# Kernel optimization log

Measured on AMD Instinct MI355X. Metric: run time of the kernel, lower is better.

## Reference

```python
import jax, jax.numpy as jnp
import numpy as np

NEG_INF = -9e15
ALPHA = 0.2  # attention leaky_relu slope


def _gat_layer(h, adj_mask, W, a1, a2):
    # h: [N, Fin], W: [Fin, D], a1/a2: [D]
    Wh = h @ W                                   # [N, D]
    f1 = Wh @ a1                                 # [N]
    f2 = Wh @ a2                                 # [N]
    e = jax.nn.leaky_relu(f1[:, None] + f2[None, :], ALPHA)  # [N, N]
    scores = jnp.where(adj_mask, e, NEG_INF)
    att = jax.nn.softmax(scores, axis=-1)        # row-normalized over neighbors
    return att @ Wh                              # [N, D]


def setup_inputs() -> dict:
    key = jax.random.key(0)
    ks = jax.random.split(key, 12)
    N, Fin, H, D, C = 4096, 512, 8, 64, 64
    s = 0.1
    x = jax.random.normal(ks[0], (N, Fin), jnp.float32)
    adj = jax.random.randint(ks[1], (N, N), 0, 2, jnp.int32)
    W = jax.random.normal(ks[2], (H, Fin, D), jnp.float32) * s
    a1 = jax.random.normal(ks[3], (H, D), jnp.float32) * s
    a2 = jax.random.normal(ks[4], (H, D), jnp.float32) * s
    Wo = jax.random.normal(ks[5], (H * D, C), jnp.float32) * s
    ao1 = jax.random.normal(ks[6], (C,), jnp.float32) * s
    ao2 = jax.random.normal(ks[7], (C,), jnp.float32) * s
    W1 = jax.random.normal(ks[8], (512, N), jnp.float32) * 0.01  # nn.Linear(N, 512)
    b1 = jnp.zeros((512,), jnp.float32)
    W2 = jax.random.normal(ks[9], (256, 512), jnp.float32) * 0.04  # nn.Linear(512, 256)
    b2 = jnp.zeros((256,), jnp.float32)
    return {"x": x, "adj": adj, "W": W, "a1": a1, "a2": a2,
            "Wo": Wo, "ao1": ao1, "ao2": ao2,
            "W1": W1, "b1": b1, "W2": W2, "b2": b2}


def reference(x, adj, W, a1, a2, Wo, ao1, ao2, W1, b1, W2, b2):
    mask = adj > 0                                    # [N, N]
    # multi-head dense attention, concat=True -> ELU per head
    heads = jax.vmap(lambda Wk, a1k, a2k: _gat_layer(x, mask, Wk, a1k, a2k))(W, a1, a2)  # [H, N, D]
    h = jax.nn.elu(heads).transpose(1, 0, 2).reshape(x.shape[0], -1)  # [N, H*D]
    # output attention layer, concat=False (no inner ELU), then outer ELU
    out = jax.nn.elu(_gat_layer(h, mask, Wo, ao1, ao2))  # [N, C]
    out = jax.nn.log_softmax(out, axis=0)                # over nodes (dim=0)
    # MLP head on transposed features: [C, N] -> [C, 512] -> [C, 256]
    y = jax.nn.leaky_relu(out.T @ W1.T + b1, 0.1)
    y = y @ W2.T + b2
    return y
```

## Files before the change

kernel.cpp:

```cpp
#include <hip/hip_runtime.h>
#include <hip/hip_bf16.h>
#include <math.h>


#define N_NODES 4096
#define FIN 512
#define NHEAD 8
#define DHEAD 64
#define NCLS 64
#define NW 64

typedef unsigned short u16;
typedef unsigned long long u64;
typedef __attribute__((ext_vector_type(8))) short bf16x8;
typedef __attribute__((ext_vector_type(4))) float f32x4;

__device__ __forceinline__ float lrelu02(float x) { return x > 0.f ? x : 0.2f * x; }
__device__ __forceinline__ u16 bf16u(float x) {
    __hip_bfloat16 h = __float2bfloat16(x);
    return __builtin_bit_cast(unsigned short, h);
}
__device__ __forceinline__ f32x4 mfma16(bf16x8 a, bf16x8 b, f32x4 c) {
    return __builtin_amdgcn_mfma_f32_16x16x32_bf16(a, b, c, 0, 0, 0);
}
__device__ __forceinline__ unsigned fkey(float f) {
    unsigned u = __builtin_bit_cast(unsigned, f);
    return (u & 0x80000000u) ? ~u : (u | 0x80000000u);
}
__device__ __forceinline__ float funkey(unsigned k) {
    unsigned u = (k & 0x80000000u) ? (k ^ 0x80000000u) : ~k;
    return __builtin_bit_cast(float, u);
}

__global__ void pack_mask(const int* __restrict__ adj, u64* __restrict__ mb,
                          unsigned* __restrict__ gmk) {
    if (blockIdx.x == 0 && threadIdx.x < 16) gmk[threadIdx.x] = 0u;
    int nwaves = (gridDim.x * blockDim.x) >> 6;
    int wid = (blockIdx.x * blockDim.x + threadIdx.x) >> 6;
    int lane = threadIdx.x & 63;
    for (int w = wid; w < N_NODES * NW; w += nwaves) {
        int i = w >> 6, wc = w & 63;
        int j = (wc << 6) | lane;
        u64 m = __ballot(adj[(size_t)i * N_NODES + j] > 0);
        if (lane == 0) mb[w] = m;
    }
}

__global__ void cvt4b(const float* __restrict__ sa, u16* __restrict__ da, int n4a,
                      const float* __restrict__ sb, u16* __restrict__ db, int n4b) {
    int i = blockIdx.x * blockDim.x + threadIdx.x;
    const float* s;
    u16* d;
    if (i < n4a) { s = sa; d = da; }
    else { i -= n4a; if (i >= n4b) return; s = sb; d = db; }
    float4 v = ((const float4*)s)[i];
    ushort4 o = {bf16u(v.x), bf16u(v.y), bf16u(v.z), bf16u(v.w)};
    ((ushort4*)d)[i] = o;
}

__global__ __launch_bounds__(256) void wT9(
    const float* __restrict__ W, const float* __restrict__ Wo,
    u16* __restrict__ WBt, u16* __restrict__ WoBt) {
    __shared__ alignas(16) u16 T[64][72];
    const int y = blockIdx.y;
    const float* src = (y < 8) ? W + (size_t)y * FIN * DHEAD : Wo;
    u16* d = (y < 8) ? WBt + (size_t)y * DHEAD * FIN : WoBt;
    const int j0 = blockIdx.x * 64;
    const int t = threadIdx.x;
    const int row = t & 63, g = t >> 6;
    #pragma unroll
    for (int k = 0; k < 16; k += 4) {
        float4 v = *(const float4*)(src + (size_t)(j0 + row) * 64 + g * 16 + k);
        T[g * 16 + k + 0][row] = bf16u(v.x);
        T[g * 16 + k + 1][row] = bf16u(v.y);
        T[g * 16 + k + 2][row] = bf16u(v.z);
        T[g * 16 + k + 3][row] = bf16u(v.w);
    }
    __syncthreads();
    const int dd = t >> 2, jc = (t & 3) * 16;
    *(uint4*)(d + (size_t)dd * FIN + j0 + jc) = *(const uint4*)&T[dd][jc];
    *(uint4*)(d + (size_t)dd * FIN + j0 + jc + 8) = *(const uint4*)&T[dd][jc + 8];
}

__global__ __launch_bounds__(256) void gemm_fused(
    const u16* __restrict__ A, int lda, const u16* __restrict__ Bt, int ldb,
    const float* __restrict__ a1a, const float* __restrict__ a2a,
    u16* __restrict__ WhBT, float* __restrict__ f1o, float* __restrict__ f2o,
    unsigned* __restrict__ gmk, int K) {
    __shared__ alignas(16) u16 T[64][72];
    const int t = threadIdx.x, lane = t & 63, wv = t >> 6;
    const int c16 = lane & 15, kg = lane >> 4;
    const int h = blockIdx.x;
    const int bm = blockIdx.y * 64;
    const u16* Ap = A + (size_t)(bm + wv * 16 + c16) * lda + kg * 8;
    const u16* Bp = Bt + (size_t)(h * 64 + c16) * ldb + kg * 8;
    f32x4 acc[4] = {};
    #pragma unroll 4
    for (int k0 = 0; k0 < K; k0 += 32) {
        bf16x8 a = *(const bf16x8*)(Ap + k0);
        #pragma unroll
        for (int ct = 0; ct < 4; ++ct) {
            bf16x8 b = *(const bf16x8*)(Bp + (size_t)ct * 16 * ldb + k0);
            acc[ct] = mfma16(a, b, acc[ct]);
        }
    }
    float a1v[4], a2v[4];
    #pragma unroll
    for (int ct = 0; ct < 4; ++ct) {
        a1v[ct] = a1a[h * 64 + ct * 16 + c16];
        a2v[ct] = a2a[h * 64 + ct * 16 + c16];
    }
    float mx = -1e30f;
    #pragma unroll
    for (int r = 0; r < 4; ++r) {
        float s1 = 0.f, s2 = 0.f;
        int rl = wv * 16 + kg * 4 + r;
        #pragma unroll
        for (int ct = 0; ct < 4; ++ct) {
            float v = acc[ct][r];
            s1 = fmaf(v, a1v[ct], s1);
            s2 = fmaf(v, a2v[ct], s2);
            T[ct * 16 + c16][rl] = bf16u(v);
        }
        #pragma unroll
        for (int off = 1; off < 16; off <<= 1) {
            s1 += __shfl_xor(s1, off, 64);
            s2 += __shfl_xor(s2, off, 64);
        }
        if (c16 == 0) {
            f1o[(size_t)h * N_NODES + bm + rl] = s1;
            f2o[(size_t)h * N_NODES + bm + rl] = s2;
        }
        mx = fmaxf(mx, s2);
    }
    mx = fmaxf(mx, __shfl_xor(mx, 16, 64));
    mx = fmaxf(mx, __shfl_xor(mx, 32, 64));
    if (lane == 0) atomicMax(&gmk[h], fkey(mx));
    __syncthreads();
    const int dd = t >> 2, jc = (t & 3) * 16;
    u16* dst = WhBT + (size_t)(h * 64 + dd) * N_NODES + bm;
    *(uint4*)(dst + jc) = *(const uint4*)&T[dd][jc];
    *(uint4*)(dst + jc + 8) = *(const uint4*)&T[dd][jc + 8];
}

__global__ void coefk(const float* __restrict__ f1, const float* __restrict__ f2,
                      const unsigned* __restrict__ gmk, float4* __restrict__ rowc,
                      float2* __restrict__ uv) {
    int h = blockIdx.y;
    int i = blockIdx.x * 256 + threadIdx.x;
    float g = funkey(gmk[h]);
    float a = f1[(size_t)h * N_NODES + i];
    float s = a + g;
    float M = lrelu02(s);
    rowc[(size_t)h * N_NODES + i] = make_float4(__expf(s - M), __expf(0.2f * s - M), 0.f, 0.f);
    float b = f2[(size_t)h * N_NODES + i] - g;
    uv[(size_t)h * N_NODES + i] = make_float2(__expf(b), __expf(0.2f * b));
}

template <int NH, int ROWS, int JSPLIT, int OUTF>
__global__ __launch_bounds__(256) void attn_v3(
    const u16* __restrict__ WhB, const float2* __restrict__ uv,
    const float4* __restrict__ rowc, const u64* __restrict__ mb,
    float* __restrict__ outp, float* __restrict__ denP) {
    constexpr int NQ = ROWS / 4;
    constexpr int NMT = ROWS / 16;
    constexpr int NJT = (N_NODES / 64) / JSPLIT;
    __shared__ alignas(16) u16 pS[2][ROWS][64];
    __shared__ float Tof[(OUTF == 3) ? 64 * (ROWS + 1) : 1];
    const int b = blockIdx.x;
    int h, ib, js;
    if (NH == 8) { h = b & 7; int r = b >> 3; js = r % JSPLIT; ib = r / JSPLIT; }
    else { h = 0; js = b % JSPLIT; ib = b / JSPLIT; }
    const int i0 = ib * ROWS;
    const int jt0 = js * NJT;
    const int t = threadIdx.x, lane = t & 63, wv = t >> 6;
    const int wv_u = __builtin_amdgcn_readfirstlane(wv);

    const float2* __restrict__ uvp = uv + (size_t)h * N_NODES;
    const float4* __restrict__ rcp = rowc + (size_t)h * N_NODES;
    const u64* __restrict__ mbp = mb + (size_t)(i0 + wv_u) * NW + jt0;

    float Aq[NQ], Bq[NQ], den[NQ];
    #pragma unroll
    for (int q = 0; q < NQ; ++q) {
        float4 rc = rcp[i0 + q * 4 + wv];
        Aq[q] = rc.x; Bq[q] = rc.y; den[q] = 0.f;
    }
    const int wcE = lane ^ (wv << 3);
    const int wcO = lane ^ ((wv + 4) << 3);
    const int kg = lane >> 4, c16 = lane & 15;
    const int ocol = wv * 16 + c16;
    const u16* bptr = WhB + ((size_t)h * 64 + ocol) * N_NODES + jt0 * 64 + kg * 8;
    const int sw8 = (c16 & 7) << 3;
    f32x4 acc[NMT] = {};

    bf16x8 b0 = *(const bf16x8*)(bptr);
    bf16x8 b1 = *(const bf16x8*)(bptr + 32);
    float2 uvv = uvp[jt0 * 64 + lane];
    u64 m[NQ];
    #pragma unroll
    for (int q = 0; q < NQ; ++q) m[q] = mbp[q * 4 * NW];

    for (int it = 0; it < NJT; ++it) {
        const int buf = it & 1;
        const int nit = (it + 1 < NJT) ? it + 1 : it;
        bf16x8 nb0 = *(const bf16x8*)(bptr + (size_t)nit * 64);
        bf16x8 nb1 = *(const bf16x8*)(bptr + (size_t)nit * 64 + 32);
        float2 nuv = uvp[(jt0 + nit) * 64 + lane];
        u64 nm[NQ];
        #pragma unroll
        for (int q = 0; q < NQ; ++q) nm[q] = mbp[q * 4 * NW + nit];
        #pragma unroll
        for (int q = 0; q < NQ; ++q) {
            unsigned wlo = __builtin_amdgcn_readfirstlane((unsigned)m[q]);
            unsigned whi = __builtin_amdgcn_readfirstlane((unsigned)(m[q] >> 32));
            u64 ws = ((u64)whi << 32) | wlo;
            float tv = fmaxf(Aq[q] * uvv.x, Bq[q] * uvv.y);
            float p;
            asm("v_cndmask_b32 %0, 0, %1, %2" : "=v"(p) : "v"(tv), "s"(ws));
            den[q] += p;
            pS[buf][q * 4 + wv][(q & 1) ? wcO : wcE] = bf16u(p);
        }
        __syncthreads();
        __builtin_amdgcn_s_setprio(1);
        #pragma unroll
        for (int mt = 0; mt < NMT; ++mt) {
            const u16* ap = &pS[buf][mt * 16 + c16][0];
            bf16x8 a0 = *(const bf16x8*)&ap[(kg * 8) ^ sw8];
            bf16x8 a1 = *(const bf16x8*)&ap[(32 + kg * 8) ^ sw8];
            acc[mt] = mfma16(a0, b0, acc[mt]);
            acc[mt] = mfma16(a1, b1, acc[mt]);
        }
        __builtin_amdgcn_s_setprio(0);
        b0 = nb0; b1 = nb1; uvv = nuv;
        #pragma unroll
        for (int q = 0; q < NQ; ++q) m[q] = nm[q];
    }

    #pragma unroll
    for (int q = 0; q < NQ; ++q) {
        float s = den[q];
        #pragma unroll
        for (int off = 32; off; off >>= 1) s += __shfl_xor(s, off, 64);
        den[q] = s;
    }

    if constexpr (OUTF == 1) {
        if (lane == 0) {
            #pragma unroll
            for (int q = 0; q < NQ; ++q)
                denP[(size_t)js * (8 * N_NODES) + (size_t)h * N_NODES + i0 + q * 4 + wv] = den[q];
        }
        float* dst = outp + (size_t)js * N_NODES * 512;
        #pragma unroll
        for (int mt = 0; mt < NMT; ++mt)
            #pragma unroll
            for (int r = 0; r < 4; ++r)
                dst[(size_t)(i0 + mt * 16 + kg * 4 + r) * 512 + h * 64 + ocol] = acc[mt][r];
    } else {
        if (lane == 0) {
            #pragma unroll
            for (int q = 0; q < NQ; ++q)
                denP[(size_t)js * N_NODES + i0 + q * 4 + wv] = den[q];
        }
        #pragma unroll
        for (int mt = 0; mt < NMT; ++mt)
            #pragma unroll
            for (int r = 0; r < 4; ++r)
                Tof[ocol * (ROWS + 1) + mt * 16 + kg * 4 + r] = acc[mt][r];
        __syncthreads();
        const int c = t >> 2, r0 = (t & 3) * 8;
        float* dst = outp + (size_t)js * 64 * N_NODES + (size_t)c * N_NODES + i0 + r0;
        float4 v0 = {Tof[c * (ROWS + 1) + r0 + 0], Tof[c * (ROWS + 1) + r0 + 1],
                     Tof[c * (ROWS + 1) + r0 + 2], Tof[c * (ROWS + 1) + r0 + 3]};
        float4 v1 = {Tof[c * (ROWS + 1) + r0 + 4], Tof[c * (ROWS + 1) + r0 + 5],
                     Tof[c * (ROWS + 1) + r0 + 6], Tof[c * (ROWS + 1) + r0 + 7]};
        *(float4*)(dst) = v0;
        *(float4*)(dst + 4) = v1;
    }
}

__global__ __launch_bounds__(256) void combine8(
    const float* __restrict__ part, const float* __restrict__ denp,
    u16* __restrict__ hB) {
    const int t4 = (blockIdx.x * 256 + threadIdx.x) * 4;
    const int i = t4 >> 9, c = t4 & 511, h = c >> 6;
    float4 s = {0.f, 0.f, 0.f, 0.f};
    float d = 0.f;
    #pragma unroll
    for (int js = 0; js < 4; ++js) {
        float4 p = *(const float4*)(part + (size_t)js * N_NODES * 512 + t4);
        s.x += p.x; s.y += p.y; s.z += p.z; s.w += p.w;
        d += denp[(size_t)js * (8 * N_NODES) + h * N_NODES + i];
    }
    float inv = d > 0.f ? 1.f / d : 0.f;
    float v[4] = {s.x * inv, s.y * inv, s.z * inv, s.w * inv};
    ushort4 o;
    #pragma unroll
    for (int k = 0; k < 4; ++k) {
        float e = v[k] > 0.f ? v[k] : expm1f(v[k]);
        ((u16*)&o)[k] = bf16u(e);
    }
    *(ushort4*)(hB + t4) = o;
}

__global__ __launch_bounds__(256) void combine1_lsm(
    const float* __restrict__ partT, const float* __restrict__ denp,
    u16* __restrict__ lsT) {
    __shared__ float vb[N_NODES];
    __shared__ float r[256];
    const int c = blockIdx.x, t = threadIdx.x;
    float m = -1e30f;
    for (int i = t * 4; i < N_NODES; i += 1024) {
        float4 s = {0.f, 0.f, 0.f, 0.f}, d = {0.f, 0.f, 0.f, 0.f};
        #pragma unroll
        for (int js = 0; js < 8; ++js) {
            float4 pv = *(const float4*)(partT + (size_t)js * 64 * N_NODES +
                                         (size_t)c * N_NODES + i);
            float4 dv = *(const float4*)(denp + (size_t)js * N_NODES + i);
            s.x += pv.x; s.y += pv.y; s.z += pv.z; s.w += pv.w;
            d.x += dv.x; d.y += dv.y; d.z += dv.z; d.w += dv.w;
        }
        float vv[4] = {d.x > 0.f ? s.x / d.x : 0.f, d.y > 0.f ? s.y / d.y : 0.f,
                       d.z > 0.f ? s.z / d.z : 0.f, d.w > 0.f ? s.w / d.w : 0.f};
        #pragma unroll
        for (int k = 0; k < 4; ++k) {
            float e = vv[k] > 0.f ? vv[k] : expm1f(vv[k]);
            vb[i + k] = e;
            m = fmaxf(m, e);
        }
    }
    r[t] = m;
    __syncthreads();
    for (int s = 128; s; s >>= 1) {
        if (t < s) r[t] = fmaxf(r[t], r[t + s]);
        __syncthreads();
    }
    m = r[0];
    __syncthreads();
    float sum = 0.f;
    for (int i = t; i < N_NODES; i += 256) sum += __expf(vb[i] - m);
    r[t] = sum;
    __syncthreads();
    for (int s = 128; s; s >>= 1) {
        if (t < s) r[t] += r[t + s];
        __syncthreads();
    }
    float lse = m + __logf(r[0]);
    for (int i = t * 4; i < N_NODES; i += 1024) {
        ushort4 o = {bf16u(vb[i] - lse), bf16u(vb[i + 1] - lse),
                     bf16u(vb[i + 2] - lse), bf16u(vb[i + 3] - lse)};
        *(ushort4*)(lsT + (size_t)c * N_NODES + i) = o;
    }
}

__global__ __launch_bounds__(256) void mlp1_mfma(
    const u16* __restrict__ lsT, const u16* __restrict__ W1B,
    float* __restrict__ part) {
    const int t = threadIdx.x, lane = t & 63, wv = t >> 6;
    const int c16 = lane & 15, kg = lane >> 4;
    const int ks = blockIdx.x & 15;
    const int bn = (blockIdx.x >> 4) * 64;
    const int kb = ks * 256;
    const u16* Ap = lsT + (size_t)(wv * 16 + c16) * N_NODES + kb + kg * 8;
    const u16* Bp = W1B + (size_t)(bn + c16) * N_NODES + kb + kg * 8;
    f32x4 acc[4] = {};
    #pragma unroll
    for (int k0 = 0; k0 < 256; k0 += 32) {
        bf16x8 a = *(const bf16x8*)(Ap + k0);
        #pragma unroll
        for (int ct = 0; ct < 4; ++ct) {
            bf16x8 b = *(const bf16x8*)(Bp + (size_t)ct * 16 * N_NODES + k0);
            acc[ct] = mfma16(a, b, acc[ct]);
        }
    }
    float* dst = part + (size_t)ks * 64 * 512;
    #pragma unroll
    for (int ct = 0; ct < 4; ++ct)
        #pragma unroll
        for (int r = 0; r < 4; ++r)
            dst[(size_t)(wv * 16 + kg * 4 + r) * 512 + bn + ct * 16 + c16] = acc[ct][r];
}

__global__ __launch_bounds__(256) void mlp2f(
    const float* __restrict__ part, const float* __restrict__ b1,
    const float* __restrict__ W2, const float* __restrict__ b2,
    float* __restrict__ out) {
    __shared__ alignas(16) float row[512];
    const int c = blockIdx.x, t = threadIdx.x;
    #pragma unroll
    for (int half = 0; half < 2; ++half) {
        int o = t + half * 256;
        float s = 0.f;
        #pragma unroll
        for (int ks = 0; ks < 16; ++ks)
            s += part[(size_t)ks * 32768 + (size_t)c * 512 + o];
        s += b1[o];
        row[o] = s > 0.f ? s : 0.1f * s;
    }
    __syncthreads();
    float acc = 0.f;
    #pragma unroll 4
    for (int o = 0; o < 512; o += 4) {
        float4 w4 = *(const float4*)(W2 + (size_t)t * 512 + o);
        float4 r4 = *(const float4*)(&row[o]);
        acc += w4.x * r4.x + w4.y * r4.y + w4.z * r4.z + w4.w * r4.w;
    }
    out[(size_t)c * 256 + t] = acc + b2[t];
}

extern "C" void kernel_launch(void* const* d_in, const int* in_sizes, int n_in,
                              void* d_out, int out_size, void* d_ws, size_t ws_size,
                              hipStream_t stream) {
    const float* x   = (const float*)d_in[0];
    const int*   adj = (const int*)d_in[1];
    const float* W   = (const float*)d_in[2];
    const float* a1  = (const float*)d_in[3];
    const float* a2  = (const float*)d_in[4];
    const float* Wo  = (const float*)d_in[5];
    const float* ao1 = (const float*)d_in[6];
    const float* ao2 = (const float*)d_in[7];
    const float* W1  = (const float*)d_in[8];
    const float* b1  = (const float*)d_in[9];
    const float* W2  = (const float*)d_in[10];
    const float* b2  = (const float*)d_in[11];
    float* out = (float*)d_out;

    char* ws = (char*)d_ws;
    size_t off = 0;
    auto alloc = [&](size_t bytes) {
        void* p = ws + off;
        off += (bytes + 255) & ~(size_t)255;
        return p;
    };
    u64*     mb     = (u64*)alloc((size_t)N_NODES * NW * 8);
    u16*     xB     = (u16*)alloc((size_t)N_NODES * FIN * 2);
    u16*     WBt    = (u16*)alloc((size_t)NHEAD * DHEAD * FIN * 2);
    u16*     WoBt   = (u16*)alloc((size_t)DHEAD * FIN * 2);
    u16*     W1B    = (u16*)alloc((size_t)512 * N_NODES * 2);
    u16*     WhB    = (u16*)alloc((size_t)NHEAD * DHEAD * N_NODES * 2);
    u16*     WhoB   = (u16*)alloc((size_t)DHEAD * N_NODES * 2);
    u16*     hB     = (u16*)alloc((size_t)N_NODES * 512 * 2);
    float*   part8  = (float*)alloc((size_t)4 * N_NODES * 512 * 4);
    float*   den8   = (float*)alloc((size_t)4 * 8 * N_NODES * 4);
    float*   f1b    = (float*)alloc((size_t)9 * N_NODES * 4);
    float*   f2b    = (float*)alloc((size_t)9 * N_NODES * 4);
    unsigned* gmk   = (unsigned*)alloc(16 * 4);
    float4*  rowc   = (float4*)alloc((size_t)9 * N_NODES * 16);
    float2*  uvb    = (float2*)alloc((size_t)9 * N_NODES * 8);
    char*    ov     = (char*)part8;
    float*   partT1 = (float*)(ov);
    float*   den1   = (float*)(ov + ((size_t)8 << 20));
    u16*     lsT    = (u16*)(ov + ((size_t)8 << 20) + (256 << 10));
    float*   part   = (float*)(ov + ((size_t)9 << 20));
    (void)ws_size; (void)in_sizes; (void)n_in; (void)out_size;

    pack_mask<<<1024, 256, 0, stream>>>(adj, mb, gmk);
    cvt4b<<<(2 * N_NODES * FIN / 4 + 255) / 256, 256, 0, stream>>>(
        x, xB, N_NODES * FIN / 4, W1, W1B, 512 * N_NODES / 4);
    wT9<<<dim3(8, 9), 256, 0, stream>>>(W, Wo, WBt, WoBt);
    gemm_fused<<<dim3(8, 64), 256, 0, stream>>>(xB, FIN, WBt, FIN, a1, a2,
                                                WhB, f1b, f2b, gmk, FIN);
    coefk<<<dim3(16, 8), 256, 0, stream>>>(f1b, f2b, gmk, rowc, uvb);
    attn_v3<8, 64, 4, 1><<<(N_NODES / 64) * 4 * 8, 256, 0, stream>>>(
        WhB, uvb, rowc, mb, part8, den8);
    combine8<<<N_NODES * 512 / 4 / 256, 256, 0, stream>>>(part8, den8, hB);
    gemm_fused<<<dim3(1, 64), 256, 0, stream>>>(hB, 512, WoBt, FIN, ao1, ao2,
                                                WhoB, f1b + (size_t)8 * N_NODES,
                                                f2b + (size_t)8 * N_NODES, gmk + 8, FIN);
    coefk<<<dim3(16, 1), 256, 0, stream>>>(f1b + (size_t)8 * N_NODES,
                                           f2b + (size_t)8 * N_NODES, gmk + 8,
                                           rowc + (size_t)8 * N_NODES,
                                           uvb + (size_t)8 * N_NODES);
    attn_v3<1, 32, 8, 3><<<(N_NODES / 32) * 8, 256, 0, stream>>>(
        WhoB, uvb + (size_t)8 * N_NODES, rowc + (size_t)8 * N_NODES, mb, partT1, den1);
    combine1_lsm<<<64, 256, 0, stream>>>(partT1, den1, lsT);
    mlp1_mfma<<<128, 256, 0, stream>>>(lsT, W1B, part);
    mlp2f<<<64, 256, 0, stream>>>(part, b1, W2, b2, out);
}
```

Baseline: 214.4 us.

## Fuse prep kernels, transpose mask layout, compute attention denominators via MFMA

Merges the mask packing, bf16 conversion and weight transpose kernels into one prep launch. The packed adjacency mask is stored column-tile-major, so each wave loads 16 consecutive rows' mask words and the row coefficients are scalarized with readfirstlane. Softmax denominators are now computed with extra MFMAs against a ones vector instead of per-lane accumulation and shuffle reductions. The j-split for the multi-head attention drops from 4 to 2 and the output layer uses 64-row tiles, which shrinks partial buffers and the combine work. The combine-log-softmax kernel uses 1024 threads with one pass. The trade-offs are doubled MFMA count in the attention loop and fewer blocks in the attention grid.

```diff
diff --git a/kernel.cpp b/kernel.cpp
--- a/kernel.cpp
+++ b/kernel.cpp
@@ -8,7 +8,6 @@
 #define NHEAD 8
 #define DHEAD 64
 #define NCLS 64
-#define NW 64
 
 typedef unsigned short u16;
 typedef unsigned long long u64;
@@ -32,54 +31,54 @@
     return __builtin_bit_cast(float, u);
 }
 
-__global__ void pack_mask(const int* __restrict__ adj, u64* __restrict__ mb,
-                          unsigned* __restrict__ gmk) {
-    if (blockIdx.x == 0 && threadIdx.x < 16) gmk[threadIdx.x] = 0u;
-    int nwaves = (gridDim.x * blockDim.x) >> 6;
-    int wid = (blockIdx.x * blockDim.x + threadIdx.x) >> 6;
-    int lane = threadIdx.x & 63;
-    for (int w = wid; w < N_NODES * NW; w += nwaves) {
-        int i = w >> 6, wc = w & 63;
-        int j = (wc << 6) | lane;
-        u64 m = __ballot(adj[(size_t)i * N_NODES + j] > 0);
-        if (lane == 0) mb[w] = m;
-    }
-}
-
-__global__ void cvt4b(const float* __restrict__ sa, u16* __restrict__ da, int n4a,
-                      const float* __restrict__ sb, u16* __restrict__ db, int n4b) {
-    int i = blockIdx.x * blockDim.x + threadIdx.x;
-    const float* s;
-    u16* d;
-    if (i < n4a) { s = sa; d = da; }
-    else { i -= n4a; if (i >= n4b) return; s = sb; d = db; }
-    float4 v = ((const float4*)s)[i];
-    ushort4 o = {bf16u(v.x), bf16u(v.y), bf16u(v.z), bf16u(v.w)};
-    ((ushort4*)d)[i] = o;
-}
-
-__global__ __launch_bounds__(256) void wT9(
+__global__ __launch_bounds__(256) void prep(
+    const int* __restrict__ adj, u64* __restrict__ mbT, unsigned* __restrict__ gmk,
+    const float* __restrict__ x, u16* __restrict__ xB,
+    const float* __restrict__ W1, u16* __restrict__ W1B,
     const float* __restrict__ W, const float* __restrict__ Wo,
     u16* __restrict__ WBt, u16* __restrict__ WoBt) {
     __shared__ alignas(16) u16 T[64][72];
-    const int y = blockIdx.y;
-    const float* src = (y < 8) ? W + (size_t)y * FIN * DHEAD : Wo;
-    u16* d = (y < 8) ? WBt + (size_t)y * DHEAD * FIN : WoBt;
-    const int j0 = blockIdx.x * 64;
-    const int t = threadIdx.x;
-    const int row = t & 63, g = t >> 6;
-    #pragma unroll
-    for (int k = 0; k < 16; k += 4) {
-        float4 v = *(const float4*)(src + (size_t)(j0 + row) * 64 + g * 16 + k);
-        T[g * 16 + k + 0][row] = bf16u(v.x);
-        T[g * 16 + k + 1][row] = bf16u(v.y);
-        T[g * 16 + k + 2][row] = bf16u(v.z);
-        T[g * 16 + k + 3][row] = bf16u(v.w);
-    }
-    __syncthreads();
-    const int dd = t >> 2, jc = (t & 3) * 16;
-    *(uint4*)(d + (size_t)dd * FIN + j0 + jc) = *(const uint4*)&T[dd][jc];
-    *(uint4*)(d + (size_t)dd * FIN + j0 + jc + 8) = *(const uint4*)&T[dd][jc + 8];
+    const int bid = blockIdx.x, t = threadIdx.x;
+    if (bid < 1024) {
+        if (bid == 0 && t < 16) gmk[t] = 0u;
+        int nwaves = (1024 * 256) >> 6;
+        int wid = (bid * 256 + t) >> 6;
+        int lane = t & 63;
+        for (int w = wid; w < N_NODES * 64; w += nwaves) {
+            int i = w >> 6, wc = w & 63;
+            int j = (wc << 6) | lane;
+            u64 m = __ballot(adj[(size_t)i * N_NODES + j] > 0);
+            if (lane == 0) mbT[(size_t)wc * N_NODES + i] = m;
+        }
+    } else if (bid < 5120) {
+        int i = (bid - 1024) * 256 + t;
+        const float* s;
+        u16* d;
+        if (i < N_NODES * FIN / 4) { s = x; d = xB; }
+        else { i -= N_NODES * FIN / 4; s = W1; d = W1B; }
+        float4 v = ((const float4*)s)[i];
+        ushort4 o = {bf16u(v.x), bf16u(v.y), bf16u(v.z), bf16u(v.w)};
+        ((ushort4*)d)[i] = o;
+    } else {
+        int idx = bid - 5120;
+        int y = idx >> 3, xb = idx & 7;
+        const float* src = (y < 8) ? W + (size_t)y * FIN * DHEAD : Wo;
+        u16* d = (y < 8) ? WBt + (size_t)y * DHEAD * FIN : WoBt;
+        const int j0 = xb * 64;
+        const int row = t & 63, g = t >> 6;
+        #pragma unroll
+        for (int k = 0; k < 16; k += 4) {
+            float4 v = *(const float4*)(src + (size_t)(j0 + row) * 64 + g * 16 + k);
+            T[g * 16 + k + 0][row] = bf16u(v.x);
+            T[g * 16 + k + 1][row] = bf16u(v.y);
+            T[g * 16 + k + 2][row] = bf16u(v.z);
+            T[g * 16 + k + 3][row] = bf16u(v.w);
+        }
+        __syncthreads();
+        const int dd = t >> 2, jc = (t & 3) * 16;
+        *(uint4*)(d + (size_t)dd * FIN + j0 + jc) = *(const uint4*)&T[dd][jc];
+        *(uint4*)(d + (size_t)dd * FIN + j0 + jc + 8) = *(const uint4*)&T[dd][jc + 8];
+    }
 }
 
 __global__ __launch_bounds__(256) void gemm_fused(
@@ -144,7 +143,7 @@
 }
 
 __global__ void coefk(const float* __restrict__ f1, const float* __restrict__ f2,
-                      const unsigned* __restrict__ gmk, float4* __restrict__ rowc,
+                      const unsigned* __restrict__ gmk, float2* __restrict__ rowc,
                       float2* __restrict__ uv) {
     int h = blockIdx.y;
     int i = blockIdx.x * 256 + threadIdx.x;
@@ -152,17 +151,16 @@
     float a = f1[(size_t)h * N_NODES + i];
     float s = a + g;
     float M = lrelu02(s);
-    rowc[(size_t)h * N_NODES + i] = make_float4(__expf(s - M), __expf(0.2f * s - M), 0.f, 0.f);
+    rowc[(size_t)h * N_NODES + i] = make_float2(__expf(s - M), __expf(0.2f * s - M));
     float b = f2[(size_t)h * N_NODES + i] - g;
     uv[(size_t)h * N_NODES + i] = make_float2(__expf(b), __expf(0.2f * b));
 }
 
 template <int NH, int ROWS, int JSPLIT, int OUTF>
-__global__ __launch_bounds__(256) void attn_v3(
+__global__ __launch_bounds__(256) void attn_v5(
     const u16* __restrict__ WhB, const float2* __restrict__ uv,
-    const float4* __restrict__ rowc, const u64* __restrict__ mb,
+    const float2* __restrict__ rowc, const u64* __restrict__ mbT,
     float* __restrict__ outp, float* __restrict__ denP) {
-    constexpr int NQ = ROWS / 4;
     constexpr int NMT = ROWS / 16;
     constexpr int NJT = (N_NODES / 64) / JSPLIT;
     __shared__ alignas(16) u16 pS[2][ROWS][64];
@@ -177,29 +175,37 @@
     const int wv_u = __builtin_amdgcn_readfirstlane(wv);
 
     const float2* __restrict__ uvp = uv + (size_t)h * N_NODES;
-    const float4* __restrict__ rcp = rowc + (size_t)h * N_NODES;
-    const u64* __restrict__ mbp = mb + (size_t)(i0 + wv_u) * NW + jt0;
-
-    float Aq[NQ], Bq[NQ], den[NQ];
-    #pragma unroll
-    for (int q = 0; q < NQ; ++q) {
-        float4 rc = rcp[i0 + q * 4 + wv];
-        Aq[q] = rc.x; Bq[q] = rc.y; den[q] = 0.f;
-    }
-    const int wcE = lane ^ (wv << 3);
-    const int wcO = lane ^ ((wv + 4) << 3);
+
+    float Aq[16], Bq[16];
+    {
+        const float2* rcw = rowc + (size_t)h * N_NODES + i0 + wv_u * 16;
+        #pragma unroll
+        for (int q = 0; q < 16; ++q) {
+            float2 rc = rcw[q];
+            Aq[q] = __builtin_amdgcn_readfirstlane(rc.x);
+            Bq[q] = __builtin_amdgcn_readfirstlane(rc.y);
+        }
+    }
+
     const int kg = lane >> 4, c16 = lane & 15;
     const int ocol = wv * 16 + c16;
     const u16* bptr = WhB + ((size_t)h * 64 + ocol) * N_NODES + jt0 * 64 + kg * 8;
     const int sw8 = (c16 & 7) << 3;
     f32x4 acc[NMT] = {};
+    f32x4 acc_d[NMT] = {};
+    bf16x8 ones;
+    #pragma unroll
+    for (int i = 0; i < 8; ++i) ones[i] = (short)0x3F80;
 
     bf16x8 b0 = *(const bf16x8*)(bptr);
     bf16x8 b1 = *(const bf16x8*)(bptr + 32);
     float2 uvv = uvp[jt0 * 64 + lane];
-    u64 m[NQ];
-    #pragma unroll
-    for (int q = 0; q < NQ; ++q) m[q] = mbp[q * 4 * NW];
+    u64 m[16];
+    {
+        const u64* mrow = mbT + (size_t)jt0 * N_NODES + i0 + wv_u * 16;
+        #pragma unroll
+        for (int q = 0; q < 16; ++q) m[q] = mrow[q];
+    }
 
     for (int it = 0; it < NJT; ++it) {
         const int buf = it & 1;
@@ -207,19 +213,20 @@
         bf16x8 nb0 = *(const bf16x8*)(bptr + (size_t)nit * 64);
         bf16x8 nb1 = *(const bf16x8*)(bptr + (size_t)nit * 64 + 32);
         float2 nuv = uvp[(jt0 + nit) * 64 + lane];
-        u64 nm[NQ];
-        #pragma unroll
-        for (int q = 0; q < NQ; ++q) nm[q] = mbp[q * 4 * NW + nit];
-        #pragma unroll
-        for (int q = 0; q < NQ; ++q) {
+        #pragma unroll
+        for (int q = 0; q < 16; ++q) {
             unsigned wlo = __builtin_amdgcn_readfirstlane((unsigned)m[q]);
             unsigned whi = __builtin_amdgcn_readfirstlane((unsigned)(m[q] >> 32));
             u64 ws = ((u64)whi << 32) | wlo;
             float tv = fmaxf(Aq[q] * uvv.x, Bq[q] * uvv.y);
             float p;
             asm("v_cndmask_b32 %0, 0, %1, %2" : "=v"(p) : "v"(tv), "s"(ws));
-            den[q] += p;
-            pS[buf][q * 4 + wv][(q & 1) ? wcO : wcE] = bf16u(p);
+            pS[buf][wv * 16 + q][lane ^ ((q & 7) << 3)] = bf16u(p);
+        }
+        {
+            const u64* mrow = mbT + (size_t)(jt0 + nit) * N_NODES + i0 + wv_u * 16;
+            #pragma unroll
+            for (int q = 0; q < 16; ++q) m[q] = mrow[q];
         }
         __syncthreads();
         __builtin_amdgcn_s_setprio(1);
@@ -230,26 +237,21 @@
             bf16x8 a1 = *(const bf16x8*)&ap[(32 + kg * 8) ^ sw8];
             acc[mt] = mfma16(a0, b0, acc[mt]);
             acc[mt] = mfma16(a1, b1, acc[mt]);
+            acc_d[mt] = mfma16(a0, ones, acc_d[mt]);
+            acc_d[mt] = mfma16(a1, ones, acc_d[mt]);
         }
         __builtin_amdgcn_s_setprio(0);
         b0 = nb0; b1 = nb1; uvv = nuv;
-        #pragma unroll
-        for (int q = 0; q < NQ; ++q) m[q] = nm[q];
-    }
-
-    #pragma unroll
-    for (int q = 0; q < NQ; ++q) {
-        float s = den[q];
-        #pragma unroll
-        for (int off = 32; off; off >>= 1) s += __shfl_xor(s, off, 64);
-        den[q] = s;
     }
 
     if constexpr (OUTF == 1) {
-        if (lane == 0) {
+        if (wv == 0 && c16 == 0) {
             #pragma unroll
-            for (int q = 0; q < NQ; ++q)
-                denP[(size_t)js * (8 * N_NODES) + (size_t)h * N_NODES + i0 + q * 4 + wv] = den[q];
+            for (int mt = 0; mt < NMT; ++mt)
+                #pragma unroll
+                for (int r = 0; r < 4; ++r)
+                    denP[(size_t)js * (8 * N_NODES) + (size_t)h * N_NODES +
+                         i0 + mt * 16 + kg * 4 + r] = acc_d[mt][r];
         }
         float* dst = outp + (size_t)js * N_NODES * 512;
         #pragma unroll
@@ -258,10 +260,12 @@
             for (int r = 0; r < 4; ++r)
                 dst[(size_t)(i0 + mt * 16 + kg * 4 + r) * 512 + h * 64 + ocol] = acc[mt][r];
     } else {
-        if (lane == 0) {
+        if (wv == 0 && c16 == 0) {
             #pragma unroll
-            for (int q = 0; q < NQ; ++q)
-                denP[(size_t)js * N_NODES + i0 + q * 4 + wv] = den[q];
+            for (int mt = 0; mt < NMT; ++mt)
+                #pragma unroll
+                for (int r = 0; r < 4; ++r)
+                    denP[(size_t)js * N_NODES + i0 + mt * 16 + kg * 4 + r] = acc_d[mt][r];
         }
         #pragma unroll
         for (int mt = 0; mt < NMT; ++mt)
@@ -269,14 +273,14 @@
             for (int r = 0; r < 4; ++r)
                 Tof[ocol * (ROWS + 1) + mt * 16 + kg * 4 + r] = acc[mt][r];
         __syncthreads();
-        const int c = t >> 2, r0 = (t & 3) * 8;
+        const int c = t >> 2, r0 = (t & 3) * 16;
         float* dst = outp + (size_t)js * 64 * N_NODES + (size_t)c * N_NODES + i0 + r0;
-        float4 v0 = {Tof[c * (ROWS + 1) + r0 + 0], Tof[c * (ROWS + 1) + r0 + 1],
-                     Tof[c * (ROWS + 1) + r0 + 2], Tof[c * (ROWS + 1) + r0 + 3]};
-        float4 v1 = {Tof[c * (ROWS + 1) + r0 + 4], Tof[c * (ROWS + 1) + r0 + 5],
-                     Tof[c * (ROWS + 1) + r0 + 6], Tof[c * (ROWS + 1) + r0 + 7]};
-        *(float4*)(dst) = v0;
-        *(float4*)(dst + 4) = v1;
+        #pragma unroll
+        for (int k = 0; k < 16; k += 4) {
+            float4 v = {Tof[c * (ROWS + 1) + r0 + k + 0], Tof[c * (ROWS + 1) + r0 + k + 1],
+                        Tof[c * (ROWS + 1) + r0 + k + 2], Tof[c * (ROWS + 1) + r0 + k + 3]};
+            *(float4*)(dst + k) = v;
+        }
     }
 }
 
@@ -285,16 +289,12 @@
     u16* __restrict__ hB) {
     const int t4 = (blockIdx.x * 256 + threadIdx.x) * 4;
     const int i = t4 >> 9, c = t4 & 511, h = c >> 6;
-    float4 s = {0.f, 0.f, 0.f, 0.f};
-    float d = 0.f;
-    #pragma unroll
-    for (int js = 0; js < 4; ++js) {
-        float4 p = *(const float4*)(part + (size_t)js * N_NODES * 512 + t4);
-        s.x += p.x; s.y += p.y; s.z += p.z; s.w += p.w;
-        d += denp[(size_t)js * (8 * N_NODES) + h * N_NODES + i];
-    }
+    float4 p0 = *(const float4*)(part + t4);
+    float4 p1 = *(const float4*)(part + (size_t)N_NODES * 512 + t4);
+    float d = denp[h * N_NODES + i] + denp[8 * N_NODES + h * N_NODES + i];
     float inv = d > 0.f ? 1.f / d : 0.f;
-    float v[4] = {s.x * inv, s.y * inv, s.z * inv, s.w * inv};
+    float v[4] = {(p0.x + p1.x) * inv, (p0.y + p1.y) * inv,
+                  (p0.z + p1.z) * inv, (p0.w + p1.w) * inv};
     ushort4 o;
     #pragma unroll
     for (int k = 0; k < 4; ++k) {
@@ -304,54 +304,51 @@
     *(ushort4*)(hB + t4) = o;
 }
 
-__global__ __launch_bounds__(256) void combine1_lsm(
+__global__ __launch_bounds__(1024) void combine1_lsm(
     const float* __restrict__ partT, const float* __restrict__ denp,
     u16* __restrict__ lsT) {
     __shared__ float vb[N_NODES];
-    __shared__ float r[256];
+    __shared__ float r[1024];
     const int c = blockIdx.x, t = threadIdx.x;
+    const int i = t * 4;
+    float4 s = {0.f, 0.f, 0.f, 0.f}, d = {0.f, 0.f, 0.f, 0.f};
+    #pragma unroll
+    for (int js = 0; js < 8; ++js) {
+        float4 pv = *(const float4*)(partT + (size_t)js * 64 * N_NODES +
+                                     (size_t)c * N_NODES + i);
+        float4 dv = *(const float4*)(denp + (size_t)js * N_NODES + i);
+        s.x += pv.x; s.y += pv.y; s.z += pv.z; s.w += pv.w;
+        d.x += dv.x; d.y += dv.y; d.z += dv.z; d.w += dv.w;
+    }
+    float vv[4] = {d.x > 0.f ? s.x / d.x : 0.f, d.y > 0.f ? s.y / d.y : 0.f,
+                   d.z > 0.f ? s.z / d.z : 0.f, d.w > 0.f ? s.w / d.w : 0.f};
     float m = -1e30f;
-    for (int i = t * 4; i < N_NODES; i += 1024) {
-        float4 s = {0.f, 0.f, 0.f, 0.f}, d = {0.f, 0.f, 0.f, 0.f};
-        #pragma unroll
-        for (int js = 0; js < 8; ++js) {
-            float4 pv = *(const float4*)(partT + (size_t)js * 64 * N_NODES +
-                                         (size_t)c * N_NODES + i);
-            float4 dv = *(const float4*)(denp + (size_t)js * N_NODES + i);
-            s.x += pv.x; s.y += pv.y; s.z += pv.z; s.w += pv.w;
-            d.x += dv.x; d.y += dv.y; d.z += dv.z; d.w += dv.w;
-        }
-        float vv[4] = {d.x > 0.f ? s.x / d.x : 0.f, d.y > 0.f ? s.y / d.y : 0.f,
-                       d.z > 0.f ? s.z / d.z : 0.f, d.w > 0.f ? s.w / d.w : 0.f};
-        #pragma unroll
-        for (int k = 0; k < 4; ++k) {
-            float e = vv[k] > 0.f ? vv[k] : expm1f(vv[k]);
-            vb[i + k] = e;
-            m = fmaxf(m, e);
-        }
+    #pragma unroll
+    for (int k = 0; k < 4; ++k) {
+        float e = vv[k] > 0.f ? vv[k] : expm1f(vv[k]);
+        vb[i + k] = e;
+        m = fmaxf(m, e);
     }
     r[t] = m;
     __syncthreads();
-    for (int s = 128; s; s >>= 1) {
-        if (t < s) r[t] = fmaxf(r[t], r[t + s]);
+    for (int st = 512; st; st >>= 1) {
+        if (t < st) r[t] = fmaxf(r[t], r[t + st]);
         __syncthreads();
     }
     m = r[0];
     __syncthreads();
     float sum = 0.f;
-    for (int i = t; i < N_NODES; i += 256) sum += __expf(vb[i] - m);
+    for (int ii = t; ii < N_NODES; ii += 1024) sum += __expf(vb[ii] - m);
     r[t] = sum;
     __syncthreads();
-    for (int s = 128; s; s >>= 1) {
-        if (t < s) r[t] += r[t + s];
+    for (int st = 512; st; st >>= 1) {
+        if (t < st) r[t] += r[t + st];
         __syncthreads();
     }
     float lse = m + __logf(r[0]);
-    for (int i = t * 4; i < N_NODES; i += 1024) {
-        ushort4 o = {bf16u(vb[i] - lse), bf16u(vb[i + 1] - lse),
-                     bf16u(vb[i + 2] - lse), bf16u(vb[i + 3] - lse)};
-        *(ushort4*)(lsT + (size_t)c * N_NODES + i) = o;
-    }
+    ushort4 o = {bf16u(vb[i] - lse), bf16u(vb[i + 1] - lse),
+                 bf16u(vb[i + 2] - lse), bf16u(vb[i + 3] - lse)};
+    *(ushort4*)(lsT + (size_t)c * N_NODES + i) = o;
 }
 
 __global__ __launch_bounds__(256) void mlp1_mfma(
@@ -433,7 +430,7 @@
         off += (bytes + 255) & ~(size_t)255;
         return p;
     };
-    u64*     mb     = (u64*)alloc((size_t)N_NODES * NW * 8);
+    u64*     mbT    = (u64*)alloc((size_t)N_NODES * 64 * 8);
     u16*     xB     = (u16*)alloc((size_t)N_NODES * FIN * 2);
     u16*     WBt    = (u16*)alloc((size_t)NHEAD * DHEAD * FIN * 2);
     u16*     WoBt   = (u16*)alloc((size_t)DHEAD * FIN * 2);
@@ -441,12 +438,12 @@
     u16*     WhB    = (u16*)alloc((size_t)NHEAD * DHEAD * N_NODES * 2);
     u16*     WhoB   = (u16*)alloc((size_t)DHEAD * N_NODES * 2);
     u16*     hB     = (u16*)alloc((size_t)N_NODES * 512 * 2);
-    float*   part8  = (float*)alloc((size_t)4 * N_NODES * 512 * 4);
-    float*   den8   = (float*)alloc((size_t)4 * 8 * N_NODES * 4);
+    float*   part8  = (float*)alloc((size_t)2 * N_NODES * 512 * 4);
+    float*   den8   = (float*)alloc((size_t)2 * 8 * N_NODES * 4);
     float*   f1b    = (float*)alloc((size_t)9 * N_NODES * 4);
     float*   f2b    = (float*)alloc((size_t)9 * N_NODES * 4);
     unsigned* gmk   = (unsigned*)alloc(16 * 4);
-    float4*  rowc   = (float4*)alloc((size_t)9 * N_NODES * 16);
+    float2*  rowc   = (float2*)alloc((size_t)9 * N_NODES * 8);
     float2*  uvb    = (float2*)alloc((size_t)9 * N_NODES * 8);
     char*    ov     = (char*)part8;
     float*   partT1 = (float*)(ov);
@@ -455,15 +452,12 @@
     float*   part   = (float*)(ov + ((size_t)9 << 20));
     (void)ws_size; (void)in_sizes; (void)n_in; (void)out_size;
 
-    pack_mask<<<1024, 256, 0, stream>>>(adj, mb, gmk);
-    cvt4b<<<(2 * N_NODES * FIN / 4 + 255) / 256, 256, 0, stream>>>(
-        x, xB, N_NODES * FIN / 4, W1, W1B, 512 * N_NODES / 4);
-    wT9<<<dim3(8, 9), 256, 0, stream>>>(W, Wo, WBt, WoBt);
+    prep<<<5192, 256, 0, stream>>>(adj, mbT, gmk, x, xB, W1, W1B, W, Wo, WBt, WoBt);
     gemm_fused<<<dim3(8, 64), 256, 0, stream>>>(xB, FIN, WBt, FIN, a1, a2,
                                                 WhB, f1b, f2b, gmk, FIN);
     coefk<<<dim3(16, 8), 256, 0, stream>>>(f1b, f2b, gmk, rowc, uvb);
-    attn_v3<8, 64, 4, 1><<<(N_NODES / 64) * 4 * 8, 256, 0, stream>>>(
-        WhB, uvb, rowc, mb, part8, den8);
+    attn_v5<8, 64, 2, 1><<<(N_NODES / 64) * 2 * 8, 256, 0, stream>>>(
+        WhB, uvb, rowc, mbT, part8, den8);
     combine8<<<N_NODES * 512 / 4 / 256, 256, 0, stream>>>(part8, den8, hB);
     gemm_fused<<<dim3(1, 64), 256, 0, stream>>>(hB, 512, WoBt, FIN, ao1, ao2,
                                                 WhoB, f1b + (size_t)8 * N_NODES,
@@ -472,9 +466,9 @@
                                            f2b + (size_t)8 * N_NODES, gmk + 8,
                                            rowc + (size_t)8 * N_NODES,
                                            uvb + (size_t)8 * N_NODES);
-    attn_v3<1, 32, 8, 3><<<(N_NODES / 32) * 8, 256, 0, stream>>>(
-        WhoB, uvb + (size_t)8 * N_NODES, rowc + (size_t)8 * N_NODES, mb, partT1, den1);
-    combine1_lsm<<<64, 256, 0, stream>>>(partT1, den1, lsT);
+    attn_v5<1, 64, 8, 3><<<(N_NODES / 64) * 8, 256, 0, stream>>>(
+        WhoB, uvb + (size_t)8 * N_NODES, rowc + (size_t)8 * N_NODES, mbT, partT1, den1);
+    combine1_lsm<<<64, 1024, 0, stream>>>(partT1, den1, lsT);
     mlp1_mfma<<<128, 256, 0, stream>>>(lsT, W1B, part);
     mlp2f<<<64, 256, 0, stream>>>(part, b1, W2, b2, out);
 }
```

After: 213.5 us. About the same (-0.4%).

## Merge prep kernels into one launch and halve attention split-K partitions

Applied to the files above, without the earlier changes.

Combines the mask packing, bf16 conversion, and weight transpose kernels into a single prep launch that dispatches by block index. This removes two kernel launches. Separately, it halves the number of column splits in both attention kernels (4→2 and 8→4), so the combine kernels read fewer partial buffers and the workspace shrinks. The trade-off is fewer attention blocks, and with them less parallelism and longer per-block loops.

```diff
diff --git a/kernel.cpp b/kernel.cpp
--- a/kernel.cpp
+++ b/kernel.cpp
@@ -32,54 +32,54 @@
     return __builtin_bit_cast(float, u);
 }
 
-__global__ void pack_mask(const int* __restrict__ adj, u64* __restrict__ mb,
-                          unsigned* __restrict__ gmk) {
-    if (blockIdx.x == 0 && threadIdx.x < 16) gmk[threadIdx.x] = 0u;
-    int nwaves = (gridDim.x * blockDim.x) >> 6;
-    int wid = (blockIdx.x * blockDim.x + threadIdx.x) >> 6;
-    int lane = threadIdx.x & 63;
-    for (int w = wid; w < N_NODES * NW; w += nwaves) {
-        int i = w >> 6, wc = w & 63;
-        int j = (wc << 6) | lane;
-        u64 m = __ballot(adj[(size_t)i * N_NODES + j] > 0);
-        if (lane == 0) mb[w] = m;
-    }
-}
-
-__global__ void cvt4b(const float* __restrict__ sa, u16* __restrict__ da, int n4a,
-                      const float* __restrict__ sb, u16* __restrict__ db, int n4b) {
-    int i = blockIdx.x * blockDim.x + threadIdx.x;
-    const float* s;
-    u16* d;
-    if (i < n4a) { s = sa; d = da; }
-    else { i -= n4a; if (i >= n4b) return; s = sb; d = db; }
-    float4 v = ((const float4*)s)[i];
-    ushort4 o = {bf16u(v.x), bf16u(v.y), bf16u(v.z), bf16u(v.w)};
-    ((ushort4*)d)[i] = o;
-}
-
-__global__ __launch_bounds__(256) void wT9(
+__global__ __launch_bounds__(256) void prep(
+    const int* __restrict__ adj, u64* __restrict__ mb, unsigned* __restrict__ gmk,
+    const float* __restrict__ x, u16* __restrict__ xB,
+    const float* __restrict__ W1, u16* __restrict__ W1B,
     const float* __restrict__ W, const float* __restrict__ Wo,
     u16* __restrict__ WBt, u16* __restrict__ WoBt) {
     __shared__ alignas(16) u16 T[64][72];
-    const int y = blockIdx.y;
-    const float* src = (y < 8) ? W + (size_t)y * FIN * DHEAD : Wo;
-    u16* d = (y < 8) ? WBt + (size_t)y * DHEAD * FIN : WoBt;
-    const int j0 = blockIdx.x * 64;
-    const int t = threadIdx.x;
-    const int row = t & 63, g = t >> 6;
-    #pragma unroll
-    for (int k = 0; k < 16; k += 4) {
-        float4 v = *(const float4*)(src + (size_t)(j0 + row) * 64 + g * 16 + k);
-        T[g * 16 + k + 0][row] = bf16u(v.x);
-        T[g * 16 + k + 1][row] = bf16u(v.y);
-        T[g * 16 + k + 2][row] = bf16u(v.z);
-        T[g * 16 + k + 3][row] = bf16u(v.w);
-    }
-    __syncthreads();
-    const int dd = t >> 2, jc = (t & 3) * 16;
-    *(uint4*)(d + (size_t)dd * FIN + j0 + jc) = *(const uint4*)&T[dd][jc];
-    *(uint4*)(d + (size_t)dd * FIN + j0 + jc + 8) = *(const uint4*)&T[dd][jc + 8];
+    const int bid = blockIdx.x, t = threadIdx.x;
+    if (bid < 1024) {
+        if (bid == 0 && t < 16) gmk[t] = 0u;
+        int nwaves = (1024 * 256) >> 6;
+        int wid = (bid * 256 + t) >> 6;
+        int lane = t & 63;
+        for (int w = wid; w < N_NODES * NW; w += nwaves) {
+            int i = w >> 6, wc = w & 63;
+            int j = (wc << 6) | lane;
+            u64 m = __ballot(adj[(size_t)i * N_NODES + j] > 0);
+            if (lane == 0) mb[w] = m;
+        }
+    } else if (bid < 5120) {
+        int i = (bid - 1024) * 256 + t;
+        const float* s;
+        u16* d;
+        if (i < N_NODES * FIN / 4) { s = x; d = xB; }
+        else { i -= N_NODES * FIN / 4; s = W1; d = W1B; }
+        float4 v = ((const float4*)s)[i];
+        ushort4 o = {bf16u(v.x), bf16u(v.y), bf16u(v.z), bf16u(v.w)};
+        ((ushort4*)d)[i] = o;
+    } else {
+        int idx = bid - 5120;
+        int y = idx >> 3, xb = idx & 7;
+        const float* src = (y < 8) ? W + (size_t)y * FIN * DHEAD : Wo;
+        u16* d = (y < 8) ? WBt + (size_t)y * DHEAD * FIN : WoBt;
+        const int j0 = xb * 64;
+        const int row = t & 63, g = t >> 6;
+        #pragma unroll
+        for (int k = 0; k < 16; k += 4) {
+            float4 v = *(const float4*)(src + (size_t)(j0 + row) * 64 + g * 16 + k);
+            T[g * 16 + k + 0][row] = bf16u(v.x);
+            T[g * 16 + k + 1][row] = bf16u(v.y);
+            T[g * 16 + k + 2][row] = bf16u(v.z);
+            T[g * 16 + k + 3][row] = bf16u(v.w);
+        }
+        __syncthreads();
+        const int dd = t >> 2, jc = (t & 3) * 16;
+        *(uint4*)(d + (size_t)dd * FIN + j0 + jc) = *(const uint4*)&T[dd][jc];
+        *(uint4*)(d + (size_t)dd * FIN + j0 + jc + 8) = *(const uint4*)&T[dd][jc + 8];
+    }
 }
 
 __global__ __launch_bounds__(256) void gemm_fused(
@@ -285,16 +285,12 @@
     u16* __restrict__ hB) {
     const int t4 = (blockIdx.x * 256 + threadIdx.x) * 4;
     const int i = t4 >> 9, c = t4 & 511, h = c >> 6;
-    float4 s = {0.f, 0.f, 0.f, 0.f};
-    float d = 0.f;
-    #pragma unroll
-    for (int js = 0; js < 4; ++js) {
-        float4 p = *(const float4*)(part + (size_t)js * N_NODES * 512 + t4);
-        s.x += p.x; s.y += p.y; s.z += p.z; s.w += p.w;
-        d += denp[(size_t)js * (8 * N_NODES) + h * N_NODES + i];
-    }
+    float4 p0 = *(const float4*)(part + t4);
+    float4 p1 = *(const float4*)(part + (size_t)N_NODES * 512 + t4);
+    float d = denp[h * N_NODES + i] + denp[8 * N_NODES + h * N_NODES + i];
     float inv = d > 0.f ? 1.f / d : 0.f;
-    float v[4] = {s.x * inv, s.y * inv, s.z * inv, s.w * inv};
+    float v[4] = {(p0.x + p1.x) * inv, (p0.y + p1.y) * inv,
+                  (p0.z + p1.z) * inv, (p0.w + p1.w) * inv};
     ushort4 o;
     #pragma unroll
     for (int k = 0; k < 4; ++k) {
@@ -314,7 +310,7 @@
     for (int i = t * 4; i < N_NODES; i += 1024) {
         float4 s = {0.f, 0.f, 0.f, 0.f}, d = {0.f, 0.f, 0.f, 0.f};
         #pragma unroll
-        for (int js = 0; js < 8; ++js) {
+        for (int js = 0; js < 4; ++js) {
             float4 pv = *(const float4*)(partT + (size_t)js * 64 * N_NODES +
                                          (size_t)c * N_NODES + i);
             float4 dv = *(const float4*)(denp + (size_t)js * N_NODES + i);
@@ -441,8 +437,8 @@
     u16*     WhB    = (u16*)alloc((size_t)NHEAD * DHEAD * N_NODES * 2);
     u16*     WhoB   = (u16*)alloc((size_t)DHEAD * N_NODES * 2);
     u16*     hB     = (u16*)alloc((size_t)N_NODES * 512 * 2);
-    float*   part8  = (float*)alloc((size_t)4 * N_NODES * 512 * 4);
-    float*   den8   = (float*)alloc((size_t)4 * 8 * N_NODES * 4);
+    float*   part8  = (float*)alloc((size_t)2 * N_NODES * 512 * 4);
+    float*   den8   = (float*)alloc((size_t)2 * 8 * N_NODES * 4);
     float*   f1b    = (float*)alloc((size_t)9 * N_NODES * 4);
     float*   f2b    = (float*)alloc((size_t)9 * N_NODES * 4);
     unsigned* gmk   = (unsigned*)alloc(16 * 4);
@@ -450,19 +446,16 @@
     float2*  uvb    = (float2*)alloc((size_t)9 * N_NODES * 8);
     char*    ov     = (char*)part8;
     float*   partT1 = (float*)(ov);
-    float*   den1   = (float*)(ov + ((size_t)8 << 20));
-    u16*     lsT    = (u16*)(ov + ((size_t)8 << 20) + (256 << 10));
-    float*   part   = (float*)(ov + ((size_t)9 << 20));
+    float*   den1   = (float*)(ov + ((size_t)4 << 20));
+    u16*     lsT    = (u16*)(ov + ((size_t)4 << 20) + (256 << 10));
+    float*   part   = (float*)(ov + ((size_t)5 << 20));
     (void)ws_size; (void)in_sizes; (void)n_in; (void)out_size;
 
-    pack_mask<<<1024, 256, 0, stream>>>(adj, mb, gmk);
-    cvt4b<<<(2 * N_NODES * FIN / 4 + 255) / 256, 256, 0, stream>>>(
-        x, xB, N_NODES * FIN / 4, W1, W1B, 512 * N_NODES / 4);
-    wT9<<<dim3(8, 9), 256, 0, stream>>>(W, Wo, WBt, WoBt);
+    prep<<<5192, 256, 0, stream>>>(adj, mb, gmk, x, xB, W1, W1B, W, Wo, WBt, WoBt);
     gemm_fused<<<dim3(8, 64), 256, 0, stream>>>(xB, FIN, WBt, FIN, a1, a2,
                                                 WhB, f1b, f2b, gmk, FIN);
     coefk<<<dim3(16, 8), 256, 0, stream>>>(f1b, f2b, gmk, rowc, uvb);
-    attn_v3<8, 64, 4, 1><<<(N_NODES / 64) * 4 * 8, 256, 0, stream>>>(
+    attn_v3<8, 64, 2, 1><<<(N_NODES / 64) * 2 * 8, 256, 0, stream>>>(
         WhB, uvb, rowc, mb, part8, den8);
     combine8<<<N_NODES * 512 / 4 / 256, 256, 0, stream>>>(part8, den8, hB);
     gemm_fused<<<dim3(1, 64), 256, 0, stream>>>(hB, 512, WoBt, FIN, ao1, ao2,
@@ -472,7 +465,7 @@
                                            f2b + (size_t)8 * N_NODES, gmk + 8,
                                            rowc + (size_t)8 * N_NODES,
                                            uvb + (size_t)8 * N_NODES);
-    attn_v3<1, 32, 8, 3><<<(N_NODES / 32) * 8, 256, 0, stream>>>(
+    attn_v3<1, 32, 4, 3><<<(N_NODES / 32) * 4, 256, 0, stream>>>(
         WhoB, uvb + (size_t)8 * N_NODES, rowc + (size_t)8 * N_NODES, mb, partT1, den1);
     combine1_lsm<<<64, 256, 0, stream>>>(partT1, den1, lsT);
     mlp1_mfma<<<128, 256, 0, stream>>>(lsT, W1B, part);
```

Result: faster. 201.4 us (-6.1%).
